# Performance work log

Hardware: AMD Instinct MI355X
Metric: run time of the kernel (lower is better)

Reference implementation:

```python
import jax, jax.numpy as jnp
import numpy as np

B, T, F, H, C = 128, 512, 784, 256, 10
BN_EPS = 1e-3  # keras BatchNormalization default epsilon


def setup_inputs() -> dict:
    key = jax.random.key(0)
    ks = jax.random.split(key, 12)
    x = jax.random.normal(ks[0], (B, T, F), dtype=jnp.float32)
    # PeepholeLSTMCell params; keras gate order is [i, f, c, o]
    kernel = jax.random.normal(ks[1], (F, 4 * H), dtype=jnp.float32) / np.sqrt(F)
    rec_kernel = jax.random.normal(ks[2], (H, 4 * H), dtype=jnp.float32) / np.sqrt(H)
    bias = jnp.concatenate([
        jnp.zeros((H,), jnp.float32),   # i
        jnp.ones((H,), jnp.float32),    # f (unit_forget_bias=True)
        jnp.zeros((2 * H,), jnp.float32),  # c, o
    ])
    w_ci = jax.random.normal(ks[3], (H,), dtype=jnp.float32) * 0.1
    w_cf = jax.random.normal(ks[4], (H,), dtype=jnp.float32) * 0.1
    w_co = jax.random.normal(ks[5], (H,), dtype=jnp.float32) * 0.1
    # BatchNorm (inference-mode) params
    gamma = jnp.ones((H,), jnp.float32)
    beta = jnp.zeros((H,), jnp.float32)
    mov_mean = jax.random.normal(ks[6], (H,), dtype=jnp.float32) * 0.1
    mov_var = jax.random.uniform(ks[7], (H,), dtype=jnp.float32, minval=0.5, maxval=1.5)
    fc_w = jax.random.normal(ks[8], (H, C), dtype=jnp.float32) / np.sqrt(H)
    return {"x": x, "kernel": kernel, "rec_kernel": rec_kernel, "bias": bias,
            "w_ci": w_ci, "w_cf": w_cf, "w_co": w_co,
            "gamma": gamma, "beta": beta, "mov_mean": mov_mean, "mov_var": mov_var,
            "fc_w": fc_w}


def reference(x, kernel, rec_kernel, bias, w_ci, w_cf, w_co,
              gamma, beta, mov_mean, mov_var, fc_w):
    b, t, _ = x.shape
    h_dim = rec_kernel.shape[0]
    # Precompute input projection once (big GEMM): [B,T,4H]
    xw = jnp.einsum('btf,fk->btk', x, kernel) + bias

    def step(carry, xw_t):
        h, c = carry
        z = xw_t + h @ rec_kernel  # [B,4H]
        zi, zf, zc, zo = jnp.split(z, 4, axis=-1)
        i = jax.nn.sigmoid(zi + c * w_ci)        # input gate w/ peephole on c_prev
        f = jax.nn.sigmoid(zf + c * w_cf)        # forget gate w/ peephole on c_prev
        c_new = f * c + i * jnp.tanh(zc)
        o = jax.nn.sigmoid(zo + c_new * w_co)    # output gate w/ peephole on c_new
        h_new = o * jnp.tanh(c_new)
        return (h_new, c_new), h_new

    init = (jnp.zeros((b, h_dim), x.dtype), jnp.zeros((b, h_dim), x.dtype))
    _, hs = jax.lax.scan(step, init, xw.transpose(1, 0, 2))  # hs: [T,B,H]
    hs = hs.transpose(1, 0, 2).reshape(-1, h_dim)            # [B*T, H]
    # BN (inference) -> tanh -> bias-free Dense
    y = (hs - mov_mean) * jax.lax.rsqrt(mov_var + BN_EPS) * gamma + beta
    y = jnp.tanh(y)
    logits = y @ fc_w
    return logits.reshape(b, t, -1)
```

## Files before the change

### kernel.cpp

```cpp
#include <hip/hip_runtime.h>
#include <hip/hip_bf16.h>
#include <hip/hip_fp16.h>
#include <stdint.h>


typedef __attribute__((ext_vector_type(8))) short short8;
typedef __attribute__((ext_vector_type(4))) float f32x4;

__device__ __forceinline__ unsigned short f2bf(float f) {
  union { float f; uint32_t u; } v; v.f = f;
  return (unsigned short)((v.u + 0x7fffu + ((v.u >> 16) & 1u)) >> 16);
}
__device__ __forceinline__ float bfu2f(uint32_t u16) {
  union { uint32_t u; float f; } v; v.u = u16 << 16; return v.f;
}
__device__ __forceinline__ float sigm(float x) { return 1.f / (1.f + __expf(-x)); }
__device__ __forceinline__ float tanh_(float x) {
  float e = __expf(2.f * x);
  return 1.f - 2.f / (e + 1.f);
}

__global__ void repack_w(const float* __restrict__ w, unsigned short* __restrict__ wt_hi,
                         unsigned short* __restrict__ wt_lo) {
  int idx = blockIdx.x * 256 + threadIdx.x;
  if (idx >= 1024 * 800) return;
  int n = idx / 800, k = idx - n * 800;
  float v = (k < 784) ? w[k * 1024 + n] : 0.f;
  unsigned short hi = f2bf(v);
  wt_hi[idx] = hi;
  wt_lo[idx] = f2bf(v - bfu2f(hi));
}

__global__ void repack_wf(const float* __restrict__ rk, unsigned short* __restrict__ wf) {
  int idx = blockIdx.x * 256 + threadIdx.x;
  if (idx >= 32768) return;
  int lane = idx & 63, ks = (idx >> 6) & 7, G = (idx >> 9) & 3;
  int w = (idx >> 11) & 3, g = (idx >> 13) & 3;
  int ncol = G * 256 + g * 64 + 16 * w + (lane & 15);
  int kb = ks * 32 + ((lane >> 4) << 3);
  union { unsigned short s[8]; uint4 v; } u;
  #pragma unroll
  for (int e = 0; e < 8; ++e) u.s[e] = f2bf(rk[(size_t)(kb + e) * 1024 + ncol]);
  ((uint4*)wf)[idx] = u.v;
}

__global__ __launch_bounds__(256, 2) void gemm_xw(
    const float* __restrict__ x, const unsigned short* __restrict__ wt_hi,
    const unsigned short* __restrict__ wt_lo, __half* __restrict__ xw) {
  __shared__ __align__(16) unsigned short As[128][40];
  __shared__ __align__(16) unsigned short Bh[128][40];
  __shared__ __align__(16) unsigned short Bl[128][40];
  const int tid = threadIdx.x;
  const int m0 = blockIdx.y << 7;
  const int n0 = blockIdx.x << 7;
  const int lane = tid & 63, wv = tid >> 6;
  const int wr = wv >> 1, wc = wv & 1;
  const int fm = lane & 15;
  const int fkb = (lane >> 4) << 3;
  const int sr = tid >> 1, sh = (tid & 1) << 4;
  f32x4 acc[4][4];
  #pragma unroll
  for (int a = 0; a < 4; ++a)
    #pragma unroll
    for (int b = 0; b < 4; ++b) acc[a][b] = (f32x4){0.f, 0.f, 0.f, 0.f};

  const float* xsrc = x + (size_t)(m0 + sr) * 784;
  const unsigned short* bhsrc = wt_hi + (size_t)(n0 + sr) * 800;
  const unsigned short* blsrc = wt_lo + (size_t)(n0 + sr) * 800;

  for (int kt = 0; kt < 25; ++kt) {
    const int kb = (kt << 5) + sh;
    float va[16];
    if (kb + 16 <= 784) {
      const float4* s = (const float4*)(xsrc + kb);
      #pragma unroll
      for (int q = 0; q < 4; ++q) {
        float4 f = s[q];
        va[q * 4 + 0] = f.x; va[q * 4 + 1] = f.y;
        va[q * 4 + 2] = f.z; va[q * 4 + 3] = f.w;
      }
    } else {
      #pragma unroll
      for (int q = 0; q < 16; ++q) va[q] = 0.f;
    }
    uint32_t pk[8];
    #pragma unroll
    for (int q = 0; q < 8; ++q)
      pk[q] = (uint32_t)f2bf(va[2 * q]) | ((uint32_t)f2bf(va[2 * q + 1]) << 16);
    uint4* adst = (uint4*)&As[sr][sh];
    adst[0] = make_uint4(pk[0], pk[1], pk[2], pk[3]);
    adst[1] = make_uint4(pk[4], pk[5], pk[6], pk[7]);
    const uint4* bh4 = (const uint4*)(bhsrc + kb);
    const uint4* bl4 = (const uint4*)(blsrc + kb);
    uint4* bhd = (uint4*)&Bh[sr][sh];
    uint4* bld = (uint4*)&Bl[sr][sh];
    bhd[0] = bh4[0]; bhd[1] = bh4[1];
    bld[0] = bl4[0]; bld[1] = bl4[1];
    __syncthreads();

    short8 af[4], bh[4], bl[4];
    #pragma unroll
    for (int mt = 0; mt < 4; ++mt)
      af[mt] = *(const short8*)&As[(wr << 6) + (mt << 4) + fm][fkb];
    #pragma unroll
    for (int nt = 0; nt < 4; ++nt) {
      bh[nt] = *(const short8*)&Bh[(wc << 6) + (nt << 4) + fm][fkb];
      bl[nt] = *(const short8*)&Bl[(wc << 6) + (nt << 4) + fm][fkb];
    }
    #pragma unroll
    for (int mt = 0; mt < 4; ++mt)
      #pragma unroll
      for (int nt = 0; nt < 4; ++nt) {
        acc[mt][nt] = __builtin_amdgcn_mfma_f32_16x16x32_bf16(af[mt], bh[nt], acc[mt][nt], 0, 0, 0);
        acc[mt][nt] = __builtin_amdgcn_mfma_f32_16x16x32_bf16(af[mt], bl[nt], acc[mt][nt], 0, 0, 0);
      }
    __syncthreads();
  }
  const int rbase = (lane >> 4) << 2;
  #pragma unroll
  for (int mt = 0; mt < 4; ++mt)
    #pragma unroll
    for (int nt = 0; nt < 4; ++nt) {
      int col = n0 + (wc << 6) + (nt << 4) + fm;
      #pragma unroll
      for (int r = 0; r < 4; ++r) {
        int row = m0 + (wr << 6) + (mt << 4) + rbase + r;
        xw[(size_t)row * 1024 + col] = __float2half(acc[mt][nt][r]);
      }
    }
}

__global__ __launch_bounds__(256, 1) void scan_kernel(
    const unsigned short* __restrict__ wf, __half* __restrict__ xw,
    unsigned long long* __restrict__ pub,
    const float* __restrict__ bias, const float* __restrict__ wci,
    const float* __restrict__ wcf, const float* __restrict__ wco,
    const float* __restrict__ gamma, const float* __restrict__ beta,
    const float* __restrict__ mean, const float* __restrict__ var) {
  __shared__ __align__(16) unsigned short h_all[16][264];
  const int tid = threadIdx.x, lane = tid & 63, w = tid >> 6;
  const int gr = blockIdx.x & 7;
  const int g = blockIdx.x >> 3;
  const int c = lane & 15, q = lane >> 4;
  const int jj = 16 * w + c, jg = 64 * g + jj;

  short8 bw[4][8];
  {
    const unsigned short* wb = wf + (size_t)(g * 4 + w) * 16384;
    #pragma unroll
    for (int G = 0; G < 4; ++G)
      #pragma unroll
      for (int ks = 0; ks < 8; ++ks)
        bw[G][ks] = *(const short8*)(wb + (size_t)((G * 8 + ks) * 64 + lane) * 8);
  }

  const float b0 = bias[jg], b1 = bias[256 + jg], b2 = bias[512 + jg], b3 = bias[768 + jg];
  const float pci = wci[jg], pcf = wcf[jg], pco = wco[jg];
  const float bna = gamma[jg] * rsqrtf(var[jg] + 1e-3f);
  const float bnb = beta[jg] - mean[jg] * bna;
  float c2[4] = {0.f, 0.f, 0.f, 0.f};

  unsigned long long* mypub = pub + (size_t)(gr * 4 + g) * 512 + jj * 8 + q * 2;
  const size_t xbase = ((size_t)(gr * 16 + 4 * q) << 9);

  float xp[4][4];
  #pragma unroll
  for (int G = 0; G < 4; ++G)
    #pragma unroll
    for (int r = 0; r < 4; ++r)
      xp[G][r] = __half2float(xw[((xbase + ((size_t)r << 9)) << 10) + G * 256 + jg]);

  for (int s = 0; s < 512; ++s) {
    f32x4 acc[4];
    #pragma unroll
    for (int G = 0; G < 4; ++G) acc[G] = (f32x4){0.f, 0.f, 0.f, 0.f};

    if (s > 0) {
      unsigned long long vv[6];
      unsigned need = 63u;
      long cnt = 0;
      const size_t slot = (size_t)(s & 1) * 16384;
      while (need) {
        #pragma unroll
        for (int pp = 0; pp < 3; ++pp) {
          int p = (g + 1 + pp) & 3;
          #pragma unroll
          for (int u2 = 0; u2 < 2; ++u2) {
            int bit = pp * 2 + u2;
            if (need & (1u << bit)) {
              unsigned long long v = __hip_atomic_load(
                  pub + slot + (size_t)(gr * 4 + p) * 512 + 2 * tid + u2,
                  __ATOMIC_RELAXED, __HIP_MEMORY_SCOPE_AGENT);
              if ((unsigned)(v >> 32) == (unsigned)s) {
                vv[bit] = v;
                need &= ~(1u << bit);
              }
            }
          }
        }
        if (++cnt > (1L << 22)) break;
      }
      #pragma unroll
      for (int pp = 0; pp < 3; ++pp) {
        int p = (g + 1 + pp) & 3;
        #pragma unroll
        for (int u2 = 0; u2 < 2; ++u2) {
          int wid = 2 * tid + u2;
          unsigned long long v = vv[pp * 2 + u2];
          int jj2 = wid >> 3, qq = (wid >> 1) & 3, uu = wid & 1;
          int m0 = 4 * qq + 2 * uu, col = 64 * p + jj2;
          h_all[m0][col] = (unsigned short)(v & 0xffffu);
          h_all[m0 + 1][col] = (unsigned short)((v >> 16) & 0xffffu);
        }
      }
      __syncthreads();
      short8 af[8];
      #pragma unroll
      for (int ks = 0; ks < 8; ++ks)
        af[ks] = *(const short8*)&h_all[c][ks * 32 + q * 8];
      #pragma unroll
      for (int ks = 0; ks < 8; ++ks)
        #pragma unroll
        for (int G = 0; G < 4; ++G)
          acc[G] = __builtin_amdgcn_mfma_f32_16x16x32_bf16(af[ks], bw[G][ks], acc[G], 0, 0, 0);
      __syncthreads();
    }

    float hn[4];
    #pragma unroll
    for (int r = 0; r < 4; ++r) {
      float z0 = acc[0][r] + b0 + xp[0][r];
      float z1 = acc[1][r] + b1 + xp[1][r];
      float z2 = acc[2][r] + b2 + xp[2][r];
      float z3 = acc[3][r] + b3 + xp[3][r];
      float ig = sigm(z0 + c2[r] * pci);
      float fg = sigm(z1 + c2[r] * pcf);
      float cn = fg * c2[r] + ig * tanh_(z2);
      float og = sigm(z3 + cn * pco);
      float h = og * tanh_(cn);
      c2[r] = cn;
      hn[r] = h;
      if ((r & 1) && s < 511) {
        unsigned long long pv =
            ((unsigned long long)(unsigned)(s + 1) << 32) |
            (unsigned long long)(((uint32_t)f2bf(hn[r - 1])) |
                                 ((uint32_t)f2bf(hn[r]) << 16));
        __hip_atomic_store(mypub + (size_t)((s + 1) & 1) * 16384 + (r >> 1), pv,
                           __ATOMIC_RELAXED, __HIP_MEMORY_SCOPE_AGENT);
      }
    }
    #pragma unroll
    for (int r = 0; r < 4; ++r) h_all[4 * q + r][jg] = f2bf(hn[r]);
    #pragma unroll
    for (int r = 0; r < 4; ++r) {
      float y = tanh_(hn[r] * bna + bnb);
      xw[((xbase + ((size_t)r << 9) + s) << 10) + jg] = __float2half(y);
    }
    if (s < 511) {
      #pragma unroll
      for (int G = 0; G < 4; ++G)
        #pragma unroll
        for (int r = 0; r < 4; ++r)
          xp[G][r] = __half2float(
              xw[((xbase + ((size_t)r << 9) + (s + 1)) << 10) + G * 256 + jg]);
    }
  }
}

__global__ __launch_bounds__(256) void final_fc(const __half* __restrict__ xw,
                                                const float* __restrict__ fcw,
                                                float* __restrict__ out) {
  const int tid = threadIdx.x, lane = tid & 63, w = tid >> 6;
  const int wid = blockIdx.x * 4 + w;
  float fw[4][10];
  #pragma unroll
  for (int q = 0; q < 4; ++q)
    #pragma unroll
    for (int c = 0; c < 10; ++c) fw[q][c] = fcw[(lane * 4 + q) * 10 + c];
  for (int it = 0; it < 128; ++it) {
    const int row = it * 512 + wid;
    uint2 u = *(const uint2*)(xw + ((size_t)row << 10) + lane * 4);
    const __half* hp = (const __half*)&u;
    float y0 = __half2float(hp[0]), y1 = __half2float(hp[1]);
    float y2 = __half2float(hp[2]), y3 = __half2float(hp[3]);
    float p[10];
    #pragma unroll
    for (int c = 0; c < 10; ++c)
      p[c] = y0 * fw[0][c] + y1 * fw[1][c] + y2 * fw[2][c] + y3 * fw[3][c];
    #pragma unroll
    for (int off = 1; off < 64; off <<= 1)
      #pragma unroll
      for (int c = 0; c < 10; ++c) p[c] += __shfl_xor(p[c], off, 64);
    if (lane == 0) {
      #pragma unroll
      for (int c = 0; c < 10; ++c) out[(size_t)row * 10 + c] = p[c];
    }
  }
}

extern "C" void kernel_launch(void* const* d_in, const int* in_sizes, int n_in,
                              void* d_out, int out_size, void* d_ws, size_t ws_size,
                              hipStream_t stream) {
  const float* x     = (const float*)d_in[0];
  const float* kw    = (const float*)d_in[1];
  const float* rk    = (const float*)d_in[2];
  const float* bias  = (const float*)d_in[3];
  const float* wci   = (const float*)d_in[4];
  const float* wcf   = (const float*)d_in[5];
  const float* wco   = (const float*)d_in[6];
  const float* gamma = (const float*)d_in[7];
  const float* beta  = (const float*)d_in[8];
  const float* mean  = (const float*)d_in[9];
  const float* var   = (const float*)d_in[10];
  const float* fcw   = (const float*)d_in[11];
  float* out = (float*)d_out;

  char* ws = (char*)d_ws;
  __half*         xw    = (__half*)ws;
  unsigned short* wt_hi = (unsigned short*)(ws + 134217728);
  unsigned short* wt_lo = (unsigned short*)(ws + 134217728 + 1638400);
  unsigned short* wfrag = (unsigned short*)(ws + 134217728 + 3276800);
  unsigned long long* pub = (unsigned long long*)(ws + 134217728);

  repack_w<<<dim3((1024 * 800 + 255) / 256), dim3(256), 0, stream>>>(kw, wt_hi, wt_lo);
  repack_wf<<<dim3(128), dim3(256), 0, stream>>>(rk, wfrag);
  gemm_xw<<<dim3(8, 512), dim3(256), 0, stream>>>(x, wt_hi, wt_lo, xw);
  scan_kernel<<<dim3(32), dim3(256), 0, stream>>>(wfrag, xw, pub, bias,
                                                  wci, wcf, wco, gamma, beta, mean, var);
  final_fc<<<dim3(128), dim3(256), 0, stream>>>(xw, fcw, out);
}
```

Baseline: 2.327 ms.

## Split recurrent scan across two blocks per batch group with overlapped local MFMA

Each batch group of 16 rows is now handled by 2 blocks of 512 threads instead of 4 blocks of 256, each block owning 128 hidden units. Every block waits on one peer instead of three, and computes the local half of the recurrent MFMAs before polling that peer's published h. This cuts cross-block synchronisation traffic and hides some spin latency behind useful compute. The cost is more work per block, a trailing barrier each step, and explicit zeroing of the publish slots at kernel start.

```diff
diff --git a/kernel.cpp b/kernel.cpp
--- a/kernel.cpp
+++ b/kernel.cpp
@@ -35,8 +35,8 @@
   int idx = blockIdx.x * 256 + threadIdx.x;
   if (idx >= 32768) return;
   int lane = idx & 63, ks = (idx >> 6) & 7, G = (idx >> 9) & 3;
-  int w = (idx >> 11) & 3, g = (idx >> 13) & 3;
-  int ncol = G * 256 + g * 64 + 16 * w + (lane & 15);
+  int w = (idx >> 11) & 7, g = (idx >> 14) & 1;
+  int ncol = G * 256 + g * 128 + 16 * w + (lane & 15);
   int kb = ks * 32 + ((lane >> 4) << 3);
   union { unsigned short s[8]; uint4 v; } u;
   #pragma unroll
@@ -130,7 +130,7 @@
     }
 }
 
-__global__ __launch_bounds__(256, 1) void scan_kernel(
+__global__ __launch_bounds__(512, 2) void scan_kernel(
     const unsigned short* __restrict__ wf, __half* __restrict__ xw,
     unsigned long long* __restrict__ pub,
     const float* __restrict__ bias, const float* __restrict__ wci,
@@ -142,11 +142,15 @@
   const int gr = blockIdx.x & 7;
   const int g = blockIdx.x >> 3;
   const int c = lane & 15, q = lane >> 4;
-  const int jj = 16 * w + c, jg = 64 * g + jj;
+  const int jj = 16 * w + c;
+  const int jg = 128 * g + jj;
+  const int pbase = 128 - 128 * g;
+  const int ksO = 4 * g;
+  const int ksP = 4 - 4 * g;
 
   short8 bw[4][8];
   {
-    const unsigned short* wb = wf + (size_t)(g * 4 + w) * 16384;
+    const unsigned short* wb = wf + (size_t)(g * 8 + w) * 16384;
     #pragma unroll
     for (int G = 0; G < 4; ++G)
       #pragma unroll
@@ -160,7 +164,13 @@
   const float bnb = beta[jg] - mean[jg] * bna;
   float c2[4] = {0.f, 0.f, 0.f, 0.f};
 
-  unsigned long long* mypub = pub + (size_t)(gr * 4 + g) * 512 + jj * 8 + q * 2;
+  unsigned long long* mypub = pub + (size_t)(gr * 2 + g) * 1024 + jj * 8 + q * 2;
+  unsigned long long* peerb = pub + (size_t)(gr * 2 + (1 - g)) * 1024 + 2 * tid;
+  __hip_atomic_store(mypub + 0, 0ull, __ATOMIC_RELAXED, __HIP_MEMORY_SCOPE_AGENT);
+  __hip_atomic_store(mypub + 1, 0ull, __ATOMIC_RELAXED, __HIP_MEMORY_SCOPE_AGENT);
+  __hip_atomic_store(mypub + 16384, 0ull, __ATOMIC_RELAXED, __HIP_MEMORY_SCOPE_AGENT);
+  __hip_atomic_store(mypub + 16385, 0ull, __ATOMIC_RELAXED, __HIP_MEMORY_SCOPE_AGENT);
+
   const size_t xbase = ((size_t)(gr * 16 + 4 * q) << 9);
 
   float xp[4][4];
@@ -176,54 +186,42 @@
     for (int G = 0; G < 4; ++G) acc[G] = (f32x4){0.f, 0.f, 0.f, 0.f};
 
     if (s > 0) {
-      unsigned long long vv[6];
-      unsigned need = 63u;
-      long cnt = 0;
-      const size_t slot = (size_t)(s & 1) * 16384;
-      while (need) {
-        #pragma unroll
-        for (int pp = 0; pp < 3; ++pp) {
-          int p = (g + 1 + pp) & 3;
-          #pragma unroll
-          for (int u2 = 0; u2 < 2; ++u2) {
-            int bit = pp * 2 + u2;
-            if (need & (1u << bit)) {
-              unsigned long long v = __hip_atomic_load(
-                  pub + slot + (size_t)(gr * 4 + p) * 512 + 2 * tid + u2,
-                  __ATOMIC_RELAXED, __HIP_MEMORY_SCOPE_AGENT);
-              if ((unsigned)(v >> 32) == (unsigned)s) {
-                vv[bit] = v;
-                need &= ~(1u << bit);
-              }
-            }
-          }
-        }
-        if (++cnt > (1L << 22)) break;
-      }
-      #pragma unroll
-      for (int pp = 0; pp < 3; ++pp) {
-        int p = (g + 1 + pp) & 3;
-        #pragma unroll
-        for (int u2 = 0; u2 < 2; ++u2) {
-          int wid = 2 * tid + u2;
-          unsigned long long v = vv[pp * 2 + u2];
-          int jj2 = wid >> 3, qq = (wid >> 1) & 3, uu = wid & 1;
-          int m0 = 4 * qq + 2 * uu, col = 64 * p + jj2;
-          h_all[m0][col] = (unsigned short)(v & 0xffffu);
-          h_all[m0 + 1][col] = (unsigned short)((v >> 16) & 0xffffu);
-        }
-      }
-      __syncthreads();
-      short8 af[8];
-      #pragma unroll
-      for (int ks = 0; ks < 8; ++ks)
-        af[ks] = *(const short8*)&h_all[c][ks * 32 + q * 8];
-      #pragma unroll
-      for (int ks = 0; ks < 8; ++ks)
+      short8 af[4];
+      #pragma unroll
+      for (int k4 = 0; k4 < 4; ++k4)
+        af[k4] = *(const short8*)&h_all[c][(ksO + k4) * 32 + q * 8];
+      #pragma unroll
+      for (int k4 = 0; k4 < 4; ++k4)
         #pragma unroll
         for (int G = 0; G < 4; ++G)
-          acc[G] = __builtin_amdgcn_mfma_f32_16x16x32_bf16(af[ks], bw[G][ks], acc[G], 0, 0, 0);
+          acc[G] = __builtin_amdgcn_mfma_f32_16x16x32_bf16(af[k4], bw[G][ksO + k4], acc[G], 0, 0, 0);
+
+      const size_t slot = (size_t)(s & 1) * 16384;
+      unsigned long long v0, v1;
+      long cnt = 0;
+      for (;;) {
+        v0 = __hip_atomic_load(peerb + slot, __ATOMIC_RELAXED, __HIP_MEMORY_SCOPE_AGENT);
+        v1 = __hip_atomic_load(peerb + slot + 1, __ATOMIC_RELAXED, __HIP_MEMORY_SCOPE_AGENT);
+        if ((unsigned)(v0 >> 32) == (unsigned)s && (unsigned)(v1 >> 32) == (unsigned)s) break;
+        if (++cnt > (1L << 22)) break;
+      }
+      {
+        const int jj2 = tid >> 2, q2 = tid & 3;
+        const int m0 = 4 * q2, col = pbase + jj2;
+        h_all[m0 + 0][col] = (unsigned short)(v0 & 0xffffu);
+        h_all[m0 + 1][col] = (unsigned short)((v0 >> 16) & 0xffffu);
+        h_all[m0 + 2][col] = (unsigned short)(v1 & 0xffffu);
+        h_all[m0 + 3][col] = (unsigned short)((v1 >> 16) & 0xffffu);
+      }
       __syncthreads();
+      #pragma unroll
+      for (int k4 = 0; k4 < 4; ++k4)
+        af[k4] = *(const short8*)&h_all[c][(ksP + k4) * 32 + q * 8];
+      #pragma unroll
+      for (int k4 = 0; k4 < 4; ++k4)
+        #pragma unroll
+        for (int G = 0; G < 4; ++G)
+          acc[G] = __builtin_amdgcn_mfma_f32_16x16x32_bf16(af[k4], bw[G][ksP + k4], acc[G], 0, 0, 0);
     }
 
     float hn[4];
@@ -264,6 +262,7 @@
           xp[G][r] = __half2float(
               xw[((xbase + ((size_t)r << 9) + (s + 1)) << 10) + G * 256 + jg]);
     }
+    __syncthreads();
   }
 }
 
@@ -325,7 +324,7 @@
   repack_w<<<dim3((1024 * 800 + 255) / 256), dim3(256), 0, stream>>>(kw, wt_hi, wt_lo);
   repack_wf<<<dim3(128), dim3(256), 0, stream>>>(rk, wfrag);
   gemm_xw<<<dim3(8, 512), dim3(256), 0, stream>>>(x, wt_hi, wt_lo, xw);
-  scan_kernel<<<dim3(32), dim3(256), 0, stream>>>(wfrag, xw, pub, bias,
+  scan_kernel<<<dim3(16), dim3(512), 0, stream>>>(wfrag, xw, pub, bias,
                                                   wci, wcf, wco, gamma, beta, mean, var);
   final_fc<<<dim3(128), dim3(256), 0, stream>>>(xw, fcw, out);
 }
```

After: 5.813 ms. 150% more time.

## Stage recurrent weights in LDS, use raw barriers and fast reciprocals in scan

Applied to the files above, without the earlier changes.

Moves the per-block recurrent weight fragments out of registers into a 128KB LDS buffer, reading them once per MFMA in the step loop. This frees about 128 VGPRs per thread, at the cost of extra LDS reads on the latency-critical serial path. Barriers become an explicit lgkmcnt wait plus s_barrier instead of __syncthreads. Divisions in sigmoid and tanh become hardware rcp approximations. The publish slots are also zeroed at kernel start.

```diff
diff --git a/kernel.cpp b/kernel.cpp
--- a/kernel.cpp
+++ b/kernel.cpp
@@ -14,10 +14,17 @@
 __device__ __forceinline__ float bfu2f(uint32_t u16) {
   union { uint32_t u; float f; } v; v.u = u16 << 16; return v.f;
 }
-__device__ __forceinline__ float sigm(float x) { return 1.f / (1.f + __expf(-x)); }
+__device__ __forceinline__ float sigm(float x) {
+  return __builtin_amdgcn_rcpf(1.f + __expf(-x));
+}
 __device__ __forceinline__ float tanh_(float x) {
   float e = __expf(2.f * x);
-  return 1.f - 2.f / (e + 1.f);
+  return 1.f - 2.f * __builtin_amdgcn_rcpf(e + 1.f);
+}
+__device__ __forceinline__ void bar_raw() {
+  asm volatile("s_waitcnt lgkmcnt(0)" ::: "memory");
+  __builtin_amdgcn_s_barrier();
+  asm volatile("" ::: "memory");
 }
 
 __global__ void repack_w(const float* __restrict__ w, unsigned short* __restrict__ wt_hi,
@@ -138,21 +145,18 @@
     const float* __restrict__ gamma, const float* __restrict__ beta,
     const float* __restrict__ mean, const float* __restrict__ var) {
   __shared__ __align__(16) unsigned short h_all[16][264];
+  __shared__ __align__(16) uint4 wlds[8192];
   const int tid = threadIdx.x, lane = tid & 63, w = tid >> 6;
   const int gr = blockIdx.x & 7;
   const int g = blockIdx.x >> 3;
   const int c = lane & 15, q = lane >> 4;
   const int jj = 16 * w + c, jg = 64 * g + jj;
 
-  short8 bw[4][8];
   {
-    const unsigned short* wb = wf + (size_t)(g * 4 + w) * 16384;
-    #pragma unroll
-    for (int G = 0; G < 4; ++G)
-      #pragma unroll
-      for (int ks = 0; ks < 8; ++ks)
-        bw[G][ks] = *(const short8*)(wb + (size_t)((G * 8 + ks) * 64 + lane) * 8);
+    const uint4* src = (const uint4*)wf + (size_t)g * 8192;
+    for (int i = tid; i < 8192; i += 256) wlds[i] = src[i];
   }
+  const short8* wl8 = (const short8*)wlds;
 
   const float b0 = bias[jg], b1 = bias[256 + jg], b2 = bias[512 + jg], b3 = bias[768 + jg];
   const float pci = wci[jg], pcf = wcf[jg], pco = wco[jg];
@@ -161,6 +165,11 @@
   float c2[4] = {0.f, 0.f, 0.f, 0.f};
 
   unsigned long long* mypub = pub + (size_t)(gr * 4 + g) * 512 + jj * 8 + q * 2;
+  __hip_atomic_store(mypub + 0, 0ull, __ATOMIC_RELAXED, __HIP_MEMORY_SCOPE_AGENT);
+  __hip_atomic_store(mypub + 1, 0ull, __ATOMIC_RELAXED, __HIP_MEMORY_SCOPE_AGENT);
+  __hip_atomic_store(mypub + 16384, 0ull, __ATOMIC_RELAXED, __HIP_MEMORY_SCOPE_AGENT);
+  __hip_atomic_store(mypub + 16385, 0ull, __ATOMIC_RELAXED, __HIP_MEMORY_SCOPE_AGENT);
+
   const size_t xbase = ((size_t)(gr * 16 + 4 * q) << 9);
 
   float xp[4][4];
@@ -169,6 +178,8 @@
     #pragma unroll
     for (int r = 0; r < 4; ++r)
       xp[G][r] = __half2float(xw[((xbase + ((size_t)r << 9)) << 10) + G * 256 + jg]);
+
+  __syncthreads();
 
   for (int s = 0; s < 512; ++s) {
     f32x4 acc[4];
@@ -213,17 +224,17 @@
           h_all[m0 + 1][col] = (unsigned short)((v >> 16) & 0xffffu);
         }
       }
-      __syncthreads();
-      short8 af[8];
-      #pragma unroll
-      for (int ks = 0; ks < 8; ++ks)
-        af[ks] = *(const short8*)&h_all[c][ks * 32 + q * 8];
-      #pragma unroll
-      for (int ks = 0; ks < 8; ++ks)
+      bar_raw();
+      #pragma unroll
+      for (int ks = 0; ks < 8; ++ks) {
+        short8 afk = *(const short8*)&h_all[c][ks * 32 + q * 8];
         #pragma unroll
-        for (int G = 0; G < 4; ++G)
-          acc[G] = __builtin_amdgcn_mfma_f32_16x16x32_bf16(af[ks], bw[G][ks], acc[G], 0, 0, 0);
-      __syncthreads();
+        for (int G = 0; G < 4; ++G) {
+          short8 bfr = wl8[((w * 4 + G) * 8 + ks) * 64 + lane];
+          acc[G] = __builtin_amdgcn_mfma_f32_16x16x32_bf16(afk, bfr, acc[G], 0, 0, 0);
+        }
+      }
+      bar_raw();
     }
 
     float hn[4];
```

Result: faster. 2.250 ms (-3.3%).
